# Kernel tuning notes

Hardware: AMD Instinct MI355X
Metric: run time of the kernel (lower is better)

The kernel has to match this reference:

```python
import jax, jax.numpy as jnp
import numpy as np

N_NODES = 50000
N_EDGES = 600000
IN_DIM = 128
HID = 128
OUT_DIM = 40
NUM_REL = 3
LN_EPS = 1e-5


def layer_norm(x, g, b):
    mu = jnp.mean(x, axis=-1, keepdims=True)
    var = jnp.var(x, axis=-1, keepdims=True)
    return (x - mu) * jax.lax.rsqrt(var + LN_EPS) * g + b


def rgcn_conv(x, edge_index, edge_type, w_rel, w_root, bias, aggr):
    """PyG-style RGCNConv: out = x @ W_root + bias + sum_r aggr_r(x_src @ W_r)."""
    src, dst = edge_index[0], edge_index[1]
    out = x @ w_root + bias                      # [N, F_out]
    for r in range(NUM_REL):                     # small fixed relation loop
        h = x @ w_rel[r]                         # transform-then-gather: [N, F_out]
        msg = h[src]                             # [E, F_out]
        mask = (edge_type == r)[:, None]
        if aggr == 'add':
            msg = jnp.where(mask, msg, 0.0)
            agg = jax.ops.segment_sum(msg, dst, num_segments=N_NODES)
        else:  # 'max'; empty segments -> 0 (matches PyG scatter_reduce include_self=False over zeros)
            msg = jnp.where(mask, msg, -jnp.inf)
            agg = jax.ops.segment_max(msg, dst, num_segments=N_NODES)
            agg = jnp.where(jnp.isfinite(agg), agg, 0.0)
        out = out + agg
    return out


def setup_inputs() -> dict:
    key = jax.random.key(0)
    ks = jax.random.split(key, 16)
    f32 = jnp.float32
    def lin(k, fan_in, shape):
        return jax.random.normal(k, shape, dtype=f32) / np.sqrt(fan_in)
    inp = {
        'x': jax.random.normal(ks[0], (N_NODES, IN_DIM), dtype=f32),
        'edge_index': jax.random.randint(ks[1], (2, N_EDGES), 0, N_NODES),
        'edge_type': jax.random.randint(ks[2], (N_EDGES,), 0, NUM_REL),
        # conv1
        'w1_rel': lin(ks[3], IN_DIM, (NUM_REL, IN_DIM, HID)),
        'w1_root': lin(ks[4], IN_DIM, (IN_DIM, HID)),
        'b1': jnp.zeros((HID,), f32),
        'ln1_g': jnp.ones((HID,), f32), 'ln1_b': jnp.zeros((HID,), f32),
        # conv2
        'w2_rel': lin(ks[5], HID, (NUM_REL, HID, HID)),
        'w2_root': lin(ks[6], HID, (HID, HID)),
        'b2': jnp.zeros((HID,), f32),
        'ln2_g': jnp.ones((HID,), f32), 'ln2_b': jnp.zeros((HID,), f32),
        # classifier
        'cw1': lin(ks[7], HID, (HID, HID)), 'cb1': jnp.zeros((HID,), f32),
        'cln1_g': jnp.ones((HID,), f32), 'cln1_b': jnp.zeros((HID,), f32),
        'cw2': lin(ks[8], HID, (HID, HID // 2)), 'cb2': jnp.zeros((HID // 2,), f32),
        'cln2_g': jnp.ones((HID // 2,), f32), 'cln2_b': jnp.zeros((HID // 2,), f32),
        'cw3': lin(ks[9], HID // 2, (HID // 2, OUT_DIM)), 'cb3': jnp.zeros((OUT_DIM,), f32),
    }
    return inp


def reference(x, edge_index, edge_type,
              w1_rel, w1_root, b1, ln1_g, ln1_b,
              w2_rel, w2_root, b2, ln2_g, ln2_b,
              cw1, cb1, cln1_g, cln1_b,
              cw2, cb2, cln2_g, cln2_b,
              cw3, cb3):
    # eval mode: edge dropout and feature dropout are identity
    h = rgcn_conv(x, edge_index, edge_type, w1_rel, w1_root, b1, 'add')
    h = jax.nn.relu(layer_norm(h, ln1_g, ln1_b))
    x1 = h
    h = rgcn_conv(x1, edge_index, edge_type, w2_rel, w2_root, b2, 'max')
    h = jax.nn.relu(layer_norm(h, ln2_g, ln2_b))
    h = h + x1 * 0.2
    # classifier MLP
    h = jax.nn.gelu(layer_norm(h @ cw1 + cb1, cln1_g, cln1_b), approximate=False)
    h = jax.nn.gelu(layer_norm(h @ cw2 + cb2, cln2_g, cln2_b), approximate=False)
    h = h @ cw3 + cb3
    return jax.nn.log_softmax(h, axis=1)
```

## Files before the change

kernel.cpp:

```cpp
#include <hip/hip_runtime.h>
#include <hip/hip_bf16.h>
#include <math.h>


typedef __attribute__((ext_vector_type(8))) short bf16x8;
typedef __attribute__((ext_vector_type(4))) float f32x4;
typedef unsigned short ushort_t;

__device__ __forceinline__ ushort_t bf16rne(float v) {
    unsigned u = __float_as_uint(v);
    return (ushort_t)((u + 0x7FFFu + ((u >> 16) & 1u)) >> 16);
}

__device__ __forceinline__ void split_bf16(float v, ushort_t& h, ushort_t& l) {
    ushort_t hu = bf16rne(v);
    float hf = __uint_as_float((unsigned)hu << 16);
    h = hu;
    l = bf16rne(v - hf);
}

__device__ __forceinline__ float bf2f(unsigned u16) {
    return __uint_as_float(u16 << 16);
}

__device__ __forceinline__ float4 unpack_bf4(uint2 u) {
    return make_float4(bf2f(u.x & 0xFFFFu), bf2f(u.x >> 16),
                       bf2f(u.y & 0xFFFFu), bf2f(u.y >> 16));
}

__device__ __forceinline__ uint2 pack_bf4(float4 v) {
    uint2 o;
    o.x = (unsigned)bf16rne(v.x) | ((unsigned)bf16rne(v.y) << 16);
    o.y = (unsigned)bf16rne(v.z) | ((unsigned)bf16rne(v.w) << 16);
    return o;
}

__device__ __forceinline__ void conv_body128(const float* __restrict__ W,
                                             ushort_t* __restrict__ out,
                                             int idx) {
    constexpr int NCF = 8;
    constexpr size_t PST = (size_t)4 * NCF * 512;
    int l = idx & 63;
    int cf = (idx >> 6) & 7;
    int ks = idx >> 9;
    int col = cf * 16 + (l & 15);
    int k0 = ks * 32 + (l >> 4) * 8;
    size_t base = (((size_t)ks * NCF + cf) * 64 + l) * 8;
#pragma unroll
    for (int j = 0; j < 8; ++j) {
        ushort_t h, lo_;
        split_bf16(W[(size_t)(k0 + j) * 128 + col], h, lo_);
        out[base + j] = h;
        out[PST + base + j] = lo_;
    }
}

__global__ __launch_bounds__(256) void convert_all(
    const float* __restrict__ w1_root, const float* __restrict__ w1_rel,
    const float* __restrict__ w2_root, const float* __restrict__ w2_rel,
    const float* __restrict__ cw1, const float* __restrict__ cw2,
    ushort_t* __restrict__ wfb) {
    int b = blockIdx.x;
    if (b < 72) {
        const float* src;
        int slot;
        if (b < 8)       { slot = 0;              src = w1_root; }
        else if (b < 32) { int r = (b - 8) >> 3;  slot = 1 + r; src = w1_rel + (size_t)r * 16384; }
        else if (b < 40) { slot = 4;              src = w2_root; }
        else if (b < 64) { int r = (b - 40) >> 3; slot = 5 + r; src = w2_rel + (size_t)r * 16384; }
        else             { slot = 8;              src = cw1; }
        int lb = (b < 8) ? b : (b < 32) ? ((b - 8) & 7) : (b < 40) ? (b - 32)
               : (b < 64) ? ((b - 40) & 7) : (b - 64);
        conv_body128(src, wfb + (size_t)slot * 32768, lb * 256 + threadIdx.x);
    } else {
        constexpr int NCF = 4;
        constexpr size_t PST = (size_t)4 * NCF * 512;
        int idx = (b - 72) * 256 + threadIdx.x;
        ushort_t* out = wfb + (size_t)9 * 32768;
        int l = idx & 63;
        int cf = (idx >> 6) & 3;
        int ks = idx >> 8;
        int col = cf * 16 + (l & 15);
        int k0 = ks * 32 + (l >> 4) * 8;
        size_t base = (((size_t)ks * NCF + cf) * 64 + l) * 8;
#pragma unroll
        for (int j = 0; j < 8; ++j) {
            ushort_t h, lo_;
            split_bf16(cw2[(size_t)(k0 + j) * 64 + col], h, lo_);
            out[base + j] = h;
            out[PST + base + j] = lo_;
        }
    }
}

__global__ __launch_bounds__(256) void x2bf(const float* __restrict__ x,
                                            ushort_t* __restrict__ xh, int n4) {
    int g = blockIdx.x * 256 + threadIdx.x;
    if (g >= n4) return;
    float4 v = ((const float4*)x)[g];
    ((uint2*)xh)[g] = pack_bf4(v);
}

template <int NCOL, int NSEG, int FUSE>
__global__ __launch_bounds__(256, 3) void gemm_bf(
    const ushort_t* __restrict__ A0, const ushort_t* __restrict__ A1,
    const ushort_t* __restrict__ A2, const ushort_t* __restrict__ A3,
    const ushort_t* __restrict__ wfrag, const float* __restrict__ bias,
    const float* __restrict__ lng, const float* __restrict__ lnb,
    void* __restrict__ Yv, int M) {
    constexpr int NCF = NCOL / 16;
    constexpr int WF = NCOL / 32;
    constexpr int PST = 4 * NCF * 512;
    constexpr int WSEG = 2 * PST;
    constexpr int RS = NCOL * 4 + 16;
    constexpr int EPB = 64 * RS;
    constexpr int SMEM_BYTES = (EPB > 16384) ? EPB : 16384;
    __shared__ __align__(16) char smem[SMEM_BYTES];
    char (*lds)[8192] = (char(*)[8192])smem;

    const int tid = threadIdx.x;
    const int wv = tid >> 6, lane = tid & 63, l15 = lane & 15, lg = lane >> 4;
    const int rowgrp = wv >> 1, colgrp = wv & 1;
    const int row0 = blockIdx.x * 64;
    const ushort_t* As[4] = {A0, A1, A2, A3};

    f32x4 acc[2][WF];
#pragma unroll
    for (int xf = 0; xf < 2; ++xf)
#pragma unroll
        for (int wf = 0; wf < WF; ++wf) acc[xf][wf] = (f32x4){0.f, 0.f, 0.f, 0.f};

    uint4 regs[2];

    auto LOADSTAGE = [&](int ch) {
        const ushort_t* __restrict__ A = As[ch >> 1];
        int kcb = (ch & 1) * 128;
#pragma unroll
        for (int i = 0; i < 2; ++i) {
            int s = tid + i * 256;
            int r = s >> 3, c16 = s & 7;
            int gr = row0 + r;
            uint4 v = make_uint4(0u, 0u, 0u, 0u);
            if (gr < M)
                v = *(const uint4*)((const char*)A + (size_t)gr * 256 + kcb + c16 * 16);
            regs[i] = v;
        }
    };

    auto WRITESTAGE = [&](int buf) {
        char* L = lds[buf];
#pragma unroll
        for (int i = 0; i < 2; ++i) {
            int s = tid + i * 256;
            int r = s >> 3, c16 = s & 7;
            int byte = (r * 128 + c16 * 16) ^ ((r & 7) << 4);
            *(uint4*)(L + byte) = regs[i];
        }
    };

    auto COMPUTE = [&](int ch, int buf) {
        int seg = ch >> 1, half = ch & 1;
        const ushort_t* __restrict__ ws = wfrag + (size_t)seg * WSEG;
        const char* L = lds[buf];
#pragma unroll
        for (int kk = 0; kk < 2; ++kk) {
            int ks = half * 2 + kk;
            bf16x8 xh[2];
#pragma unroll
            for (int xf = 0; xf < 2; ++xf) {
                int r = rowgrp * 32 + xf * 16 + l15;
                int byte = (r * 128 + kk * 64 + lg * 16) ^ ((r & 7) << 4);
                xh[xf] = *(const bf16x8*)(L + byte);
            }
            bf16x8 wh[WF], wl[WF];
#pragma unroll
            for (int wf = 0; wf < WF; ++wf) {
                size_t off = (((size_t)ks * NCF + colgrp * WF + wf) * 64 + lane) * 8;
                wh[wf] = *(const bf16x8*)(ws + off);
                wl[wf] = *(const bf16x8*)(ws + PST + off);
            }
#pragma unroll
            for (int xf = 0; xf < 2; ++xf)
#pragma unroll
                for (int wf = 0; wf < WF; ++wf) {
                    acc[xf][wf] = __builtin_amdgcn_mfma_f32_16x16x32_bf16(
                        wh[wf], xh[xf], acc[xf][wf], 0, 0, 0);
                    acc[xf][wf] = __builtin_amdgcn_mfma_f32_16x16x32_bf16(
                        wl[wf], xh[xf], acc[xf][wf], 0, 0, 0);
                }
        }
    };

    constexpr int CH = 2 * NSEG;
    LOADSTAGE(0);
    WRITESTAGE(0);
    __syncthreads();
    for (int ch = 0; ch < CH; ++ch) {
        if (ch + 1 < CH) LOADSTAGE(ch + 1);
        COMPUTE(ch, ch & 1);
        __syncthreads();
        if (ch + 1 < CH) WRITESTAGE((ch + 1) & 1);
        __syncthreads();
    }

    {
        float4 bv[WF];
#pragma unroll
        for (int wf = 0; wf < WF; ++wf) {
            int col = colgrp * (NCOL / 2) + wf * 16 + lg * 4;
            bv[wf] = bias ? *(const float4*)(bias + col)
                          : make_float4(0.f, 0.f, 0.f, 0.f);
        }
#pragma unroll
        for (int xf = 0; xf < 2; ++xf) {
            int r = rowgrp * 32 + xf * 16 + l15;
#pragma unroll
            for (int wf = 0; wf < WF; ++wf) {
                int col = colgrp * (NCOL / 2) + wf * 16 + lg * 4;
                float4 o;
                o.x = acc[xf][wf][0] + bv[wf].x;
                o.y = acc[xf][wf][1] + bv[wf].y;
                o.z = acc[xf][wf][2] + bv[wf].z;
                o.w = acc[xf][wf][3] + bv[wf].w;
                *(float4*)(smem + r * RS + col * 4) = o;
            }
        }
    }
    __syncthreads();

    if (FUSE >= 1 && FUSE <= 3) {
        constexpr int CPT = NCOL / 4;
        int r = tid >> 2, seg = tid & 3;
        char* rp = smem + r * RS + seg * CPT * 4;
        float s = 0.f, sq = 0.f;
        float4 vv[CPT / 4];
#pragma unroll
        for (int j = 0; j < CPT / 4; ++j) {
            float4 v = *(const float4*)(rp + j * 16);
            vv[j] = v;
            s += (v.x + v.y) + (v.z + v.w);
            sq += (v.x * v.x + v.y * v.y) + (v.z * v.z + v.w * v.w);
        }
        s += __shfl_xor(s, 1, 64); sq += __shfl_xor(sq, 1, 64);
        s += __shfl_xor(s, 2, 64); sq += __shfl_xor(sq, 2, 64);
        float mu = s * (1.f / NCOL);
        float var = sq * (1.f / NCOL) - mu * mu;
        float rstd = rsqrtf(var + 1e-5f);
#pragma unroll
        for (int j = 0; j < CPT / 4; ++j) {
            int c0 = seg * CPT + j * 4;
            float4 v = vv[j];
            float4 gg = *(const float4*)(lng + c0);
            float4 bb = *(const float4*)(lnb + c0);
            float y0 = (v.x - mu) * rstd * gg.x + bb.x;
            float y1 = (v.y - mu) * rstd * gg.y + bb.y;
            float y2 = (v.z - mu) * rstd * gg.z + bb.z;
            float y3 = (v.w - mu) * rstd * gg.w + bb.w;
            if (FUSE == 1) {
                y0 = fmaxf(y0, 0.f); y1 = fmaxf(y1, 0.f);
                y2 = fmaxf(y2, 0.f); y3 = fmaxf(y3, 0.f);
            } else {
                y0 = 0.5f * y0 * (1.f + erff(y0 * 0.70710678118654752f));
                y1 = 0.5f * y1 * (1.f + erff(y1 * 0.70710678118654752f));
                y2 = 0.5f * y2 * (1.f + erff(y2 * 0.70710678118654752f));
                y3 = 0.5f * y3 * (1.f + erff(y3 * 0.70710678118654752f));
            }
            vv[j] = make_float4(y0, y1, y2, y3);
        }
        __syncthreads();
        if (FUSE == 3) {
#pragma unroll
            for (int j = 0; j < CPT / 4; ++j) *(float4*)(rp + j * 16) = vv[j];
        } else {
#pragma unroll
            for (int j = 0; j < CPT / 4; ++j) {
                int c0 = seg * CPT + j * 4;
                *(uint2*)(smem + r * RS + 2 * c0) = pack_bf4(vv[j]);
            }
        }
        __syncthreads();
    }

    if (FUSE == 4) {
        constexpr int SL = 64 * (NCOL / 8);
#pragma unroll
        for (int i = 0; i < SL / 256; ++i) {
            int slot = tid + i * 256;
            int rr = slot / (NCOL / 8), c16 = slot % (NCOL / 8);
            int gr = row0 + rr;
            if (gr < M) {
                float4 a = *(const float4*)(smem + rr * RS + c16 * 32);
                float4 b = *(const float4*)(smem + rr * RS + c16 * 32 + 16);
                uint4 o;
                uint2 pa = pack_bf4(a), pb = pack_bf4(b);
                o.x = pa.x; o.y = pa.y; o.z = pb.x; o.w = pb.y;
                *(uint4*)((char*)Yv + (size_t)gr * (NCOL * 2) + c16 * 16) = o;
            }
        }
    } else {
        constexpr int OUTB = (FUSE == 0 || FUSE == 3) ? NCOL * 4 : NCOL * 2;
        constexpr int RP = OUTB / 16;
        constexpr int SL = 64 * RP;
#pragma unroll
        for (int i = 0; i < SL / 256; ++i) {
            int slot = tid + i * 256;
            int rr = slot / RP, c16 = slot % RP;
            int gr = row0 + rr;
            if (gr < M)
                *(uint4*)((char*)Yv + (size_t)gr * OUTB + c16 * 16) =
                    *(const uint4*)(smem + rr * RS + c16 * 16);
        }
    }
}

__global__ __launch_bounds__(256, 3) void gemm_conv2(
    const ushort_t* __restrict__ X, const ushort_t* __restrict__ wfb,
    const float* __restrict__ b2, ushort_t* __restrict__ ACbf,
    ushort_t* __restrict__ H0, ushort_t* __restrict__ H1,
    ushort_t* __restrict__ H2, int M) {
    constexpr int NCF = 8, WF = 4;
    constexpr int PST = 4 * NCF * 512;
    constexpr int RS2 = 256 + 16;
    __shared__ __align__(16) char smem[16384 + 64 * RS2];
    char* Xs = smem;
    char* ep = smem + 16384;

    const int tid = threadIdx.x;
    const int wv = tid >> 6, lane = tid & 63, l15 = lane & 15, lg = lane >> 4;
    const int rowgrp = wv >> 1, colgrp = wv & 1;
    const int row0 = blockIdx.x * 64;

#pragma unroll
    for (int i = 0; i < 4; ++i) {
        int s = tid + i * 256;
        int r = s >> 4, c16 = s & 15;
        int gr = row0 + r;
        uint4 v = make_uint4(0u, 0u, 0u, 0u);
        if (gr < M) v = *(const uint4*)((const char*)X + (size_t)gr * 256 + c16 * 16);
        int byte = (r * 256 + c16 * 16) ^ ((r & 7) << 4);
        *(uint4*)(Xs + byte) = v;
    }
    __syncthreads();

    ushort_t* outs[4] = {ACbf, H0, H1, H2};
    for (int set = 0; set < 4; ++set) {
        const ushort_t* __restrict__ ws = wfb + (size_t)(4 + set) * 32768;
        f32x4 acc[2][WF];
#pragma unroll
        for (int xf = 0; xf < 2; ++xf)
#pragma unroll
            for (int wf = 0; wf < WF; ++wf) acc[xf][wf] = (f32x4){0.f, 0.f, 0.f, 0.f};
#pragma unroll
        for (int ks = 0; ks < 4; ++ks) {
            bf16x8 xh[2];
#pragma unroll
            for (int xf = 0; xf < 2; ++xf) {
                int r = rowgrp * 32 + xf * 16 + l15;
                int byte = (r * 256 + ks * 64 + lg * 16) ^ ((r & 7) << 4);
                xh[xf] = *(const bf16x8*)(Xs + byte);
            }
            bf16x8 wh[WF], wl[WF];
#pragma unroll
            for (int wf = 0; wf < WF; ++wf) {
                size_t off = (((size_t)ks * NCF + colgrp * WF + wf) * 64 + lane) * 8;
                wh[wf] = *(const bf16x8*)(ws + off);
                wl[wf] = *(const bf16x8*)(ws + PST + off);
            }
#pragma unroll
            for (int xf = 0; xf < 2; ++xf)
#pragma unroll
                for (int wf = 0; wf < WF; ++wf) {
                    acc[xf][wf] = __builtin_amdgcn_mfma_f32_16x16x32_bf16(
                        wh[wf], xh[xf], acc[xf][wf], 0, 0, 0);
                    acc[xf][wf] = __builtin_amdgcn_mfma_f32_16x16x32_bf16(
                        wl[wf], xh[xf], acc[xf][wf], 0, 0, 0);
                }
        }
        __syncthreads();
#pragma unroll
        for (int xf = 0; xf < 2; ++xf) {
            int r = rowgrp * 32 + xf * 16 + l15;
#pragma unroll
            for (int wf = 0; wf < WF; ++wf) {
                int col = colgrp * 64 + wf * 16 + lg * 4;
                float4 o;
                o.x = acc[xf][wf][0];
                o.y = acc[xf][wf][1];
                o.z = acc[xf][wf][2];
                o.w = acc[xf][wf][3];
                if (set == 0) {
                    float4 bv = *(const float4*)(b2 + col);
                    o.x += bv.x; o.y += bv.y; o.z += bv.z; o.w += bv.w;
                }
                *(uint2*)(ep + r * RS2 + col * 2) = pack_bf4(o);
            }
        }
        __syncthreads();
        ushort_t* O = outs[set];
#pragma unroll
        for (int i = 0; i < 4; ++i) {
            int slot = tid + i * 256;
            int rr = slot >> 4, c16 = slot & 15;
            int gr = row0 + rr;
            if (gr < M)
                *(uint4*)((char*)O + (size_t)gr * 256 + c16 * 16) =
                    *(const uint4*)(ep + rr * RS2 + c16 * 16);
        }
    }
}

__global__ __launch_bounds__(256) void hist3_kernel(const int* __restrict__ edst,
                                                    const int* __restrict__ etype,
                                                    int* __restrict__ deg3, int E) {
    int e = blockIdx.x * 256 + threadIdx.x;
    if (e < E) atomicAdd(&deg3[edst[e] * 3 + etype[e]], 1);
}

__global__ __launch_bounds__(256) void degtot_kernel(const int* __restrict__ deg3,
                                                     int* __restrict__ degtot, int N) {
    int n = blockIdx.x * 256 + threadIdx.x;
    if (n < N) degtot[n] = deg3[n * 3] + deg3[n * 3 + 1] + deg3[n * 3 + 2];
}

__global__ __launch_bounds__(256) void scan_block(const int* __restrict__ in,
                                                  int* __restrict__ out,
                                                  int* __restrict__ sums, int n) {
    __shared__ int s[256];
    int g = blockIdx.x * 256 + threadIdx.x;
    int v = (g < n) ? in[g] : 0;
    s[threadIdx.x] = v;
    __syncthreads();
    int acc = v;
    for (int off = 1; off < 256; off <<= 1) {
        int t = (threadIdx.x >= off) ? s[threadIdx.x - off] : 0;
        __syncthreads();
        acc += t;
        s[threadIdx.x] = acc;
        __syncthreads();
    }
    if (g < n) out[g] = acc - v;
    if (threadIdx.x == 255 && sums) sums[blockIdx.x] = acc;
}

__global__ __launch_bounds__(256) void scan_add(int* __restrict__ out,
                                                const int* __restrict__ topex,
                                                int n, int total) {
    int g = blockIdx.x * 256 + threadIdx.x;
    if (g < n) out[g] += topex[blockIdx.x];
    if (g == 0) out[n] = total;
}

__global__ __launch_bounds__(256) void ranges_kernel(
    const int* __restrict__ rowptr, const int* __restrict__ deg3,
    int4* __restrict__ ranges, int* __restrict__ cursor3, int N) {
    int n = blockIdx.x * 256 + threadIdx.x;
    if (n >= N) return;
    int b = rowptr[n];
    int d0 = deg3[n * 3], d1 = deg3[n * 3 + 1];
    int4 r;
    r.x = b; r.y = b + d0; r.z = b + d0 + d1; r.w = rowptr[n + 1];
    ranges[n] = r;
    cursor3[n * 3] = r.x; cursor3[n * 3 + 1] = r.y; cursor3[n * 3 + 2] = r.z;
}

__global__ __launch_bounds__(256) void fill3_kernel(
    const int* __restrict__ esrc, const int* __restrict__ edst,
    const int* __restrict__ etype, int* __restrict__ cursor3,
    int* __restrict__ colidx, int E) {
    int e = blockIdx.x * 256 + threadIdx.x;
    if (e >= E) return;
    int pos = atomicAdd(&cursor3[edst[e] * 3 + etype[e]], 1);
    colidx[pos] = esrc[e];
}

__device__ __forceinline__ float4 gather_sum_bf(const ushort_t* __restrict__ XH,
                                                const int* __restrict__ colidx,
                                                int beg, int end, int l) {
    float4 a = make_float4(0.f, 0.f, 0.f, 0.f);
    int e = beg;
    for (; e + 4 <= end; e += 4) {
        int s0 = colidx[e], s1 = colidx[e + 1];
        int s2 = colidx[e + 2], s3 = colidx[e + 3];
        float4 v0 = unpack_bf4(*(const uint2*)(XH + (size_t)s0 * 128 + l * 4));
        float4 v1 = unpack_bf4(*(const uint2*)(XH + (size_t)s1 * 128 + l * 4));
        float4 v2 = unpack_bf4(*(const uint2*)(XH + (size_t)s2 * 128 + l * 4));
        float4 v3 = unpack_bf4(*(const uint2*)(XH + (size_t)s3 * 128 + l * 4));
        a.x += (v0.x + v1.x) + (v2.x + v3.x);
        a.y += (v0.y + v1.y) + (v2.y + v3.y);
        a.z += (v0.z + v1.z) + (v2.z + v3.z);
        a.w += (v0.w + v1.w) + (v2.w + v3.w);
    }
    for (; e < end; ++e) {
        float4 v = unpack_bf4(*(const uint2*)(XH + (size_t)colidx[e] * 128 + l * 4));
        a.x += v.x; a.y += v.y; a.z += v.z; a.w += v.w;
    }
    return a;
}

__global__ __launch_bounds__(256) void agg3_add(
    const ushort_t* __restrict__ xh, const int4* __restrict__ ranges,
    const int* __restrict__ colidx, ushort_t* __restrict__ S0,
    ushort_t* __restrict__ S1, ushort_t* __restrict__ S2, int N) {
    int node = blockIdx.x * 8 + (threadIdx.x >> 5);
    int l = threadIdx.x & 31;
    if (node >= N) return;
    int4 rg = ranges[node];
    float4 a0 = gather_sum_bf(xh, colidx, rg.x, rg.y, l);
    float4 a1 = gather_sum_bf(xh, colidx, rg.y, rg.z, l);
    float4 a2 = gather_sum_bf(xh, colidx, rg.z, rg.w, l);
    *(uint2*)(S0 + (size_t)node * 128 + l * 4) = pack_bf4(a0);
    *(uint2*)(S1 + (size_t)node * 128 + l * 4) = pack_bf4(a1);
    *(uint2*)(S2 + (size_t)node * 128 + l * 4) = pack_bf4(a2);
}

__device__ __forceinline__ float4 gather_max_bf(const ushort_t* __restrict__ H,
                                                const int* __restrict__ colidx,
                                                int beg, int end, int l) {
    float4 m = make_float4(-INFINITY, -INFINITY, -INFINITY, -INFINITY);
    int e = beg;
    for (; e + 4 <= end; e += 4) {
        int s0 = colidx[e], s1 = colidx[e + 1];
        int s2 = colidx[e + 2], s3 = colidx[e + 3];
        float4 v0 = unpack_bf4(*(const uint2*)(H + (size_t)s0 * 128 + l * 4));
        float4 v1 = unpack_bf4(*(const uint2*)(H + (size_t)s1 * 128 + l * 4));
        float4 v2 = unpack_bf4(*(const uint2*)(H + (size_t)s2 * 128 + l * 4));
        float4 v3 = unpack_bf4(*(const uint2*)(H + (size_t)s3 * 128 + l * 4));
        m.x = fmaxf(m.x, fmaxf(fmaxf(v0.x, v1.x), fmaxf(v2.x, v3.x)));
        m.y = fmaxf(m.y, fmaxf(fmaxf(v0.y, v1.y), fmaxf(v2.y, v3.y)));
        m.z = fmaxf(m.z, fmaxf(fmaxf(v0.z, v1.z), fmaxf(v2.z, v3.z)));
        m.w = fmaxf(m.w, fmaxf(fmaxf(v0.w, v1.w), fmaxf(v2.w, v3.w)));
    }
    for (; e < end; ++e) {
        float4 v = unpack_bf4(*(const uint2*)(H + (size_t)colidx[e] * 128 + l * 4));
        m.x = fmaxf(m.x, v.x); m.y = fmaxf(m.y, v.y);
        m.z = fmaxf(m.z, v.z); m.w = fmaxf(m.w, v.w);
    }
    m.x = (m.x > -3e38f) ? m.x : 0.f;
    m.y = (m.y > -3e38f) ? m.y : 0.f;
    m.z = (m.z > -3e38f) ? m.z : 0.f;
    m.w = (m.w > -3e38f) ? m.w : 0.f;
    return m;
}

__global__ __launch_bounds__(256) void maxagg_ln(
    const ushort_t* __restrict__ H0, const ushort_t* __restrict__ H1,
    const ushort_t* __restrict__ H2, const int4* __restrict__ ranges,
    const int* __restrict__ colidx, const ushort_t* __restrict__ accbf,
    const ushort_t* __restrict__ resid, const float* __restrict__ g,
    const float* __restrict__ b, ushort_t* __restrict__ outH, int N) {
    int node = blockIdx.x * 8 + (threadIdx.x >> 5);
    int l = threadIdx.x & 31;
    if (node >= N) return;
    int4 rg = ranges[node];
    float4 m0 = gather_max_bf(H0, colidx, rg.x, rg.y, l);
    float4 m1 = gather_max_bf(H1, colidx, rg.y, rg.z, l);
    float4 m2 = gather_max_bf(H2, colidx, rg.z, rg.w, l);
    float4 a = unpack_bf4(*(const uint2*)(accbf + (size_t)node * 128 + l * 4));
    a.x += m0.x + m1.x + m2.x;
    a.y += m0.y + m1.y + m2.y;
    a.z += m0.z + m1.z + m2.z;
    a.w += m0.w + m1.w + m2.w;
    float s = (a.x + a.y) + (a.z + a.w);
    float sq = (a.x * a.x + a.y * a.y) + (a.z * a.z + a.w * a.w);
#pragma unroll
    for (int off = 16; off; off >>= 1) {
        s += __shfl_xor(s, off, 64);
        sq += __shfl_xor(sq, off, 64);
    }
    float mu = s * (1.f / 128.f);
    float var = sq * (1.f / 128.f) - mu * mu;
    float rstd = rsqrtf(var + 1e-5f);
    float4 gg = *(const float4*)(g + l * 4);
    float4 bb = *(const float4*)(b + l * 4);
    float4 rv = unpack_bf4(*(const uint2*)(resid + (size_t)node * 128 + l * 4));
    float4 y;
    y.x = fmaxf((a.x - mu) * rstd * gg.x + bb.x, 0.f) + 0.2f * rv.x;
    y.y = fmaxf((a.y - mu) * rstd * gg.y + bb.y, 0.f) + 0.2f * rv.y;
    y.z = fmaxf((a.z - mu) * rstd * gg.z + bb.z, 0.f) + 0.2f * rv.z;
    y.w = fmaxf((a.w - mu) * rstd * gg.w + bb.w, 0.f) + 0.2f * rv.w;
    *(uint2*)(outH + (size_t)node * 128 + l * 4) = pack_bf4(y);
}

__global__ __launch_bounds__(256) void gemm40_lsm(const float* __restrict__ X,
                                                  const float* __restrict__ W,
                                                  const float* __restrict__ bias,
                                                  float* __restrict__ Y, int M) {
    __shared__ float Xs[64][65];
    __shared__ float Ws[64 * 40];
    __shared__ float Ys[64][41];
    __shared__ float mx_[64], ls_[64];
    const int tid = threadIdx.x;
    const int row0 = blockIdx.x * 64;
    for (int i = tid; i < 64 * 40; i += 256) Ws[i] = W[i];
#pragma unroll
    for (int i = 0; i < 4; ++i) {
        int slot = tid + i * 256;
        int r = slot >> 4, c4 = slot & 15;
        float4 v = make_float4(0.f, 0.f, 0.f, 0.f);
        if (row0 + r < M) v = *(const float4*)(X + (size_t)(row0 + r) * 64 + c4 * 4);
        Xs[r][c4 * 4 + 0] = v.x; Xs[r][c4 * 4 + 1] = v.y;
        Xs[r][c4 * 4 + 2] = v.z; Xs[r][c4 * 4 + 3] = v.w;
    }
    __syncthreads();
    const int row = tid >> 2, cg = (tid & 3) * 10;
    float acc[10];
#pragma unroll
    for (int j = 0; j < 10; ++j) acc[j] = 0.f;
#pragma unroll 8
    for (int k = 0; k < 64; ++k) {
        float xv = Xs[row][k];
#pragma unroll
        for (int j = 0; j < 10; ++j) acc[j] = fmaf(xv, Ws[k * 40 + cg + j], acc[j]);
    }
#pragma unroll
    for (int j = 0; j < 10; ++j) Ys[row][cg + j] = acc[j] + bias[cg + j];
    __syncthreads();
    if (tid < 64) {
        float mx = -INFINITY;
#pragma unroll 8
        for (int c = 0; c < 40; ++c) mx = fmaxf(mx, Ys[tid][c]);
        float sum = 0.f;
#pragma unroll 8
        for (int c = 0; c < 40; ++c) sum += __expf(Ys[tid][c] - mx);
        mx_[tid] = mx;
        ls_[tid] = logf(sum);
    }
    __syncthreads();
#pragma unroll
    for (int i = 0; i < 10; ++i) {
        int slot = tid + i * 256;
        int r = slot / 40, c = slot % 40;
        int gr = row0 + r;
        if (gr < M) Y[(size_t)gr * 40 + c] = Ys[r][c] - mx_[r] - ls_[r];
    }
}

extern "C" void kernel_launch(void* const* d_in, const int* in_sizes, int n_in,
                              void* d_out, int out_size, void* d_ws, size_t ws_size,
                              hipStream_t stream) {
    const float* x       = (const float*)d_in[0];
    const int*   eidx    = (const int*)d_in[1];
    const int*   etype   = (const int*)d_in[2];
    const float* w1_rel  = (const float*)d_in[3];
    const float* w1_root = (const float*)d_in[4];
    const float* b1      = (const float*)d_in[5];
    const float* ln1_g   = (const float*)d_in[6];
    const float* ln1_b   = (const float*)d_in[7];
    const float* w2_rel  = (const float*)d_in[8];
    const float* w2_root = (const float*)d_in[9];
    const float* b2      = (const float*)d_in[10];
    const float* ln2_g   = (const float*)d_in[11];
    const float* ln2_b   = (const float*)d_in[12];
    const float* cw1     = (const float*)d_in[13];
    const float* cb1     = (const float*)d_in[14];
    const float* cln1_g  = (const float*)d_in[15];
    const float* cln1_b  = (const float*)d_in[16];
    const float* cw2     = (const float*)d_in[17];
    const float* cb2     = (const float*)d_in[18];
    const float* cln2_g  = (const float*)d_in[19];
    const float* cln2_b  = (const float*)d_in[20];
    const float* cw3     = (const float*)d_in[21];
    const float* cb3     = (const float*)d_in[22];

    const int N = in_sizes[0] / 128;
    const int E = in_sizes[1] / 2;
    const int* esrc = eidx;
    const int* edst = eidx + E;

    const size_t HB = (size_t)N * 256;
    char* base = (char*)d_ws;
    ushort_t* S0 = (ushort_t*)(base + 0 * HB);
    ushort_t* S1 = (ushort_t*)(base + 1 * HB);
    ushort_t* S2 = (ushort_t*)(base + 2 * HB);
    ushort_t* X1 = (ushort_t*)(base + 3 * HB);
    ushort_t* AC = (ushort_t*)(base + 4 * HB);
    char*     B3 = base + 5 * HB;

    int* rowptr  = (int*)B3;
    int* degtot  = rowptr + (N + 1);
    int* deg3    = degtot + N;
    int* cursor3 = deg3 + 3 * N;
    int* bsums   = cursor3 + 3 * N;
    int* btop    = bsums + 256;
    int4* ranges = (int4*)(((uintptr_t)(btop + 256) + 15) & ~(uintptr_t)15);
    int* colidx  = (int*)(ranges + N);
    ushort_t* wfb = (ushort_t*)(((uintptr_t)(colidx + E) + 255) & ~(uintptr_t)255);
    auto WSLOT = [&](int i) { return wfb + (size_t)i * 32768; };
    ushort_t* xh = (ushort_t*)(((uintptr_t)(wfb + 10 * 32768) + 255) & ~(uintptr_t)255);
    ushort_t* h2 = xh;
    ushort_t* C1 = S0;
    float*    C2 = (float*)S1;

    const dim3 blk(256);
    const int gGemm = (N + 63) / 64;
    const int gAgg  = (N + 7) / 8;
    const int gEdge = (E + 255) / 256;
    const int gNode = (N + 255) / 256;
    const int nScanB = (N + 255) / 256;
    const int gX2  = (N * 32 + 255) / 256;

    hipMemsetAsync(deg3, 0, (size_t)3 * N * sizeof(int), stream);
    hist3_kernel<<<gEdge, blk, 0, stream>>>(edst, etype, deg3, E);
    degtot_kernel<<<gNode, blk, 0, stream>>>(deg3, degtot, N);
    scan_block<<<nScanB, blk, 0, stream>>>(degtot, rowptr, bsums, N);
    scan_block<<<1, blk, 0, stream>>>(bsums, btop, nullptr, nScanB);
    scan_add<<<nScanB, blk, 0, stream>>>(rowptr, btop, N, E);
    ranges_kernel<<<gNode, blk, 0, stream>>>(rowptr, deg3, ranges, cursor3, N);
    fill3_kernel<<<gEdge, blk, 0, stream>>>(esrc, edst, etype, cursor3, colidx, E);

    convert_all<<<76, blk, 0, stream>>>(w1_root, w1_rel, w2_root, w2_rel,
                                        cw1, cw2, wfb);
    x2bf<<<gX2, blk, 0, stream>>>(x, xh, N * 32);

    agg3_add<<<gAgg, blk, 0, stream>>>(xh, ranges, colidx, S0, S1, S2, N);
    gemm_bf<128, 4, 1><<<gGemm, blk, 0, stream>>>(
        xh, S0, S1, S2, WSLOT(0), b1, ln1_g, ln1_b, X1, N);

    gemm_conv2<<<gGemm, blk, 0, stream>>>(X1, wfb, b2, AC, S0, S1, S2, N);
    maxagg_ln<<<gAgg, blk, 0, stream>>>(S0, S1, S2, ranges, colidx, AC,
                                        X1, ln2_g, ln2_b, h2, N);

    gemm_bf<128, 1, 2><<<gGemm, blk, 0, stream>>>(
        h2, h2, h2, h2, WSLOT(8), cb1, cln1_g, cln1_b, C1, N);
    gemm_bf<64, 1, 3><<<gGemm, blk, 0, stream>>>(
        C1, C1, C1, C1, WSLOT(9), cb2, cln2_g, cln2_b, C2, N);
    gemm40_lsm<<<gGemm, blk, 0, stream>>>(C2, cw3, cb3, (float*)d_out, N);
}
```

Measured before the change: 266.9 us.

## Fuse CSR-build and conversion kernels; merge per-relation gathers into one 8-wide loop

Folds the degree sum into the block scan, merges scan_add with the ranges kernel, and merges weight conversion with the x-to-bf16 cast, which removes several small launches. The add and max aggregation kernels now walk a node's whole edge range in a single loop with 8 loads in flight, using predicates to route each edge to its relation's accumulator. The aim is more memory-level parallelism and fewer short loops per node. Max aggregation assumes S0, S1 and S2 are contiguous with stride N*128, and the predicated accumulation costs extra ALU work per edge.

```diff
diff --git a/kernel.cpp b/kernel.cpp
--- a/kernel.cpp
+++ b/kernel.cpp
@@ -55,12 +55,21 @@
     }
 }
 
-__global__ __launch_bounds__(256) void convert_all(
+__global__ __launch_bounds__(256) void convert_all_x2bf(
     const float* __restrict__ w1_root, const float* __restrict__ w1_rel,
     const float* __restrict__ w2_root, const float* __restrict__ w2_rel,
     const float* __restrict__ cw1, const float* __restrict__ cw2,
-    ushort_t* __restrict__ wfb) {
+    ushort_t* __restrict__ wfb,
+    const float* __restrict__ x, ushort_t* __restrict__ xh, int n4) {
     int b = blockIdx.x;
+    if (b >= 76) {
+        int g = (b - 76) * 256 + threadIdx.x;
+        if (g < n4) {
+            float4 v = ((const float4*)x)[g];
+            ((uint2*)xh)[g] = pack_bf4(v);
+        }
+        return;
+    }
     if (b < 72) {
         const float* src;
         int slot;
@@ -93,14 +102,6 @@
     }
 }
 
-__global__ __launch_bounds__(256) void x2bf(const float* __restrict__ x,
-                                            ushort_t* __restrict__ xh, int n4) {
-    int g = blockIdx.x * 256 + threadIdx.x;
-    if (g >= n4) return;
-    float4 v = ((const float4*)x)[g];
-    ((uint2*)xh)[g] = pack_bf4(v);
-}
-
 template <int NCOL, int NSEG, int FUSE>
 __global__ __launch_bounds__(256, 3) void gemm_bf(
     const ushort_t* __restrict__ A0, const ushort_t* __restrict__ A1,
@@ -416,10 +417,25 @@
     if (e < E) atomicAdd(&deg3[edst[e] * 3 + etype[e]], 1);
 }
 
-__global__ __launch_bounds__(256) void degtot_kernel(const int* __restrict__ deg3,
-                                                     int* __restrict__ degtot, int N) {
-    int n = blockIdx.x * 256 + threadIdx.x;
-    if (n < N) degtot[n] = deg3[n * 3] + deg3[n * 3 + 1] + deg3[n * 3 + 2];
+__global__ __launch_bounds__(256) void scan_deg3(const int* __restrict__ deg3,
+                                                 int* __restrict__ out,
+                                                 int* __restrict__ sums, int n) {
+    __shared__ int s[256];
+    int g = blockIdx.x * 256 + threadIdx.x;
+    int v = 0;
+    if (g < n) v = deg3[g * 3] + deg3[g * 3 + 1] + deg3[g * 3 + 2];
+    s[threadIdx.x] = v;
+    __syncthreads();
+    int acc = v;
+    for (int off = 1; off < 256; off <<= 1) {
+        int t = (threadIdx.x >= off) ? s[threadIdx.x - off] : 0;
+        __syncthreads();
+        acc += t;
+        s[threadIdx.x] = acc;
+        __syncthreads();
+    }
+    if (g < n) out[g] = acc - v;
+    if (threadIdx.x == 255 && sums) sums[blockIdx.x] = acc;
 }
 
 __global__ __launch_bounds__(256) void scan_block(const int* __restrict__ in,
@@ -442,25 +458,18 @@
     if (threadIdx.x == 255 && sums) sums[blockIdx.x] = acc;
 }
 
-__global__ __launch_bounds__(256) void scan_add(int* __restrict__ out,
-                                                const int* __restrict__ topex,
-                                                int n, int total) {
+__global__ __launch_bounds__(256) void scan_add_ranges(
+    const int* __restrict__ scanned, const int* __restrict__ topex,
+    const int* __restrict__ deg3, int4* __restrict__ ranges,
+    int* __restrict__ cursor3, int n) {
     int g = blockIdx.x * 256 + threadIdx.x;
-    if (g < n) out[g] += topex[blockIdx.x];
-    if (g == 0) out[n] = total;
-}
-
-__global__ __launch_bounds__(256) void ranges_kernel(
-    const int* __restrict__ rowptr, const int* __restrict__ deg3,
-    int4* __restrict__ ranges, int* __restrict__ cursor3, int N) {
-    int n = blockIdx.x * 256 + threadIdx.x;
-    if (n >= N) return;
-    int b = rowptr[n];
-    int d0 = deg3[n * 3], d1 = deg3[n * 3 + 1];
+    if (g >= n) return;
+    int b = scanned[g] + topex[blockIdx.x];
+    int d0 = deg3[g * 3], d1 = deg3[g * 3 + 1], d2 = deg3[g * 3 + 2];
     int4 r;
-    r.x = b; r.y = b + d0; r.z = b + d0 + d1; r.w = rowptr[n + 1];
-    ranges[n] = r;
-    cursor3[n * 3] = r.x; cursor3[n * 3 + 1] = r.y; cursor3[n * 3 + 2] = r.z;
+    r.x = b; r.y = b + d0; r.z = b + d0 + d1; r.w = b + d0 + d1 + d2;
+    ranges[g] = r;
+    cursor3[g * 3] = r.x; cursor3[g * 3 + 1] = r.y; cursor3[g * 3 + 2] = r.z;
 }
 
 __global__ __launch_bounds__(256) void fill3_kernel(
@@ -473,30 +482,6 @@
     colidx[pos] = esrc[e];
 }
 
-__device__ __forceinline__ float4 gather_sum_bf(const ushort_t* __restrict__ XH,
-                                                const int* __restrict__ colidx,
-                                                int beg, int end, int l) {
-    float4 a = make_float4(0.f, 0.f, 0.f, 0.f);
-    int e = beg;
-    for (; e + 4 <= end; e += 4) {
-        int s0 = colidx[e], s1 = colidx[e + 1];
-        int s2 = colidx[e + 2], s3 = colidx[e + 3];
-        float4 v0 = unpack_bf4(*(const uint2*)(XH + (size_t)s0 * 128 + l * 4));
-        float4 v1 = unpack_bf4(*(const uint2*)(XH + (size_t)s1 * 128 + l * 4));
-        float4 v2 = unpack_bf4(*(const uint2*)(XH + (size_t)s2 * 128 + l * 4));
-        float4 v3 = unpack_bf4(*(const uint2*)(XH + (size_t)s3 * 128 + l * 4));
-        a.x += (v0.x + v1.x) + (v2.x + v3.x);
-        a.y += (v0.y + v1.y) + (v2.y + v3.y);
-        a.z += (v0.z + v1.z) + (v2.z + v3.z);
-        a.w += (v0.w + v1.w) + (v2.w + v3.w);
-    }
-    for (; e < end; ++e) {
-        float4 v = unpack_bf4(*(const uint2*)(XH + (size_t)colidx[e] * 128 + l * 4));
-        a.x += v.x; a.y += v.y; a.z += v.z; a.w += v.w;
-    }
-    return a;
-}
-
 __global__ __launch_bounds__(256) void agg3_add(
     const ushort_t* __restrict__ xh, const int4* __restrict__ ranges,
     const int* __restrict__ colidx, ushort_t* __restrict__ S0,
@@ -505,46 +490,56 @@
     int l = threadIdx.x & 31;
     if (node >= N) return;
     int4 rg = ranges[node];
-    float4 a0 = gather_sum_bf(xh, colidx, rg.x, rg.y, l);
-    float4 a1 = gather_sum_bf(xh, colidx, rg.y, rg.z, l);
-    float4 a2 = gather_sum_bf(xh, colidx, rg.z, rg.w, l);
+    float4 a0 = make_float4(0.f, 0.f, 0.f, 0.f);
+    float4 a1 = a0, a2 = a0;
+    int e = rg.x, end = rg.w;
+
+    auto acc1 = [&](int ee, uint2 u) {
+        float4 v = unpack_bf4(u);
+        bool i0 = ee < rg.y;
+        bool i2 = ee >= rg.z;
+        bool i1 = !i0 && !i2;
+        a0.x += i0 ? v.x : 0.f; a0.y += i0 ? v.y : 0.f;
+        a0.z += i0 ? v.z : 0.f; a0.w += i0 ? v.w : 0.f;
+        a1.x += i1 ? v.x : 0.f; a1.y += i1 ? v.y : 0.f;
+        a1.z += i1 ? v.z : 0.f; a1.w += i1 ? v.w : 0.f;
+        a2.x += i2 ? v.x : 0.f; a2.y += i2 ? v.y : 0.f;
+        a2.z += i2 ? v.z : 0.f; a2.w += i2 ? v.w : 0.f;
+    };
+
+    for (; e + 8 <= end; e += 8) {
+        int s[8];
+#pragma unroll
+        for (int k = 0; k < 8; ++k) s[k] = colidx[e + k];
+        uint2 u[8];
+#pragma unroll
+        for (int k = 0; k < 8; ++k)
+            u[k] = *(const uint2*)(xh + (size_t)s[k] * 128 + l * 4);
+#pragma unroll
+        for (int k = 0; k < 8; ++k) acc1(e + k, u[k]);
+    }
+    if (e + 4 <= end) {
+        int s[4];
+#pragma unroll
+        for (int k = 0; k < 4; ++k) s[k] = colidx[e + k];
+        uint2 u[4];
+#pragma unroll
+        for (int k = 0; k < 4; ++k)
+            u[k] = *(const uint2*)(xh + (size_t)s[k] * 128 + l * 4);
+#pragma unroll
+        for (int k = 0; k < 4; ++k) acc1(e + k, u[k]);
+        e += 4;
+    }
+    for (; e < end; ++e)
+        acc1(e, *(const uint2*)(xh + (size_t)colidx[e] * 128 + l * 4));
+
     *(uint2*)(S0 + (size_t)node * 128 + l * 4) = pack_bf4(a0);
     *(uint2*)(S1 + (size_t)node * 128 + l * 4) = pack_bf4(a1);
     *(uint2*)(S2 + (size_t)node * 128 + l * 4) = pack_bf4(a2);
 }
 
-__device__ __forceinline__ float4 gather_max_bf(const ushort_t* __restrict__ H,
-                                                const int* __restrict__ colidx,
-                                                int beg, int end, int l) {
-    float4 m = make_float4(-INFINITY, -INFINITY, -INFINITY, -INFINITY);
-    int e = beg;
-    for (; e + 4 <= end; e += 4) {
-        int s0 = colidx[e], s1 = colidx[e + 1];
-        int s2 = colidx[e + 2], s3 = colidx[e + 3];
-        float4 v0 = unpack_bf4(*(const uint2*)(H + (size_t)s0 * 128 + l * 4));
-        float4 v1 = unpack_bf4(*(const uint2*)(H + (size_t)s1 * 128 + l * 4));
-        float4 v2 = unpack_bf4(*(const uint2*)(H + (size_t)s2 * 128 + l * 4));
-        float4 v3 = unpack_bf4(*(const uint2*)(H + (size_t)s3 * 128 + l * 4));
-        m.x = fmaxf(m.x, fmaxf(fmaxf(v0.x, v1.x), fmaxf(v2.x, v3.x)));
-        m.y = fmaxf(m.y, fmaxf(fmaxf(v0.y, v1.y), fmaxf(v2.y, v3.y)));
-        m.z = fmaxf(m.z, fmaxf(fmaxf(v0.z, v1.z), fmaxf(v2.z, v3.z)));
-        m.w = fmaxf(m.w, fmaxf(fmaxf(v0.w, v1.w), fmaxf(v2.w, v3.w)));
-    }
-    for (; e < end; ++e) {
-        float4 v = unpack_bf4(*(const uint2*)(H + (size_t)colidx[e] * 128 + l * 4));
-        m.x = fmaxf(m.x, v.x); m.y = fmaxf(m.y, v.y);
-        m.z = fmaxf(m.z, v.z); m.w = fmaxf(m.w, v.w);
-    }
-    m.x = (m.x > -3e38f) ? m.x : 0.f;
-    m.y = (m.y > -3e38f) ? m.y : 0.f;
-    m.z = (m.z > -3e38f) ? m.z : 0.f;
-    m.w = (m.w > -3e38f) ? m.w : 0.f;
-    return m;
-}
-
 __global__ __launch_bounds__(256) void maxagg_ln(
-    const ushort_t* __restrict__ H0, const ushort_t* __restrict__ H1,
-    const ushort_t* __restrict__ H2, const int4* __restrict__ ranges,
+    const ushort_t* __restrict__ Hbase, const int4* __restrict__ ranges,
     const int* __restrict__ colidx, const ushort_t* __restrict__ accbf,
     const ushort_t* __restrict__ resid, const float* __restrict__ g,
     const float* __restrict__ b, ushort_t* __restrict__ outH, int N) {
@@ -552,9 +547,59 @@
     int l = threadIdx.x & 31;
     if (node >= N) return;
     int4 rg = ranges[node];
-    float4 m0 = gather_max_bf(H0, colidx, rg.x, rg.y, l);
-    float4 m1 = gather_max_bf(H1, colidx, rg.y, rg.z, l);
-    float4 m2 = gather_max_bf(H2, colidx, rg.z, rg.w, l);
+    const float NI = -INFINITY;
+    float4 m0 = make_float4(NI, NI, NI, NI);
+    float4 m1 = m0, m2 = m0;
+    int e = rg.x, end = rg.w;
+
+    auto acc1 = [&](int ee, uint2 u) {
+        float4 v = unpack_bf4(u);
+        bool i0 = ee < rg.y;
+        bool i2 = ee >= rg.z;
+        bool i1 = !i0 && !i2;
+        m0.x = fmaxf(m0.x, i0 ? v.x : NI); m0.y = fmaxf(m0.y, i0 ? v.y : NI);
+        m0.z = fmaxf(m0.z, i0 ? v.z : NI); m0.w = fmaxf(m0.w, i0 ? v.w : NI);
+        m1.x = fmaxf(m1.x, i1 ? v.x : NI); m1.y = fmaxf(m1.y, i1 ? v.y : NI);
+        m1.z = fmaxf(m1.z, i1 ? v.z : NI); m1.w = fmaxf(m1.w, i1 ? v.w : NI);
+        m2.x = fmaxf(m2.x, i2 ? v.x : NI); m2.y = fmaxf(m2.y, i2 ? v.y : NI);
+        m2.z = fmaxf(m2.z, i2 ? v.z : NI); m2.w = fmaxf(m2.w, i2 ? v.w : NI);
+    };
+    auto addr = [&](int ee, int src) {
+        int rel = (ee >= rg.y) + (ee >= rg.z);
+        return Hbase + ((size_t)rel * N + src) * 128 + l * 4;
+    };
+
+    for (; e + 8 <= end; e += 8) {
+        int s[8];
+#pragma unroll
+        for (int k = 0; k < 8; ++k) s[k] = colidx[e + k];
+        uint2 u[8];
+#pragma unroll
+        for (int k = 0; k < 8; ++k) u[k] = *(const uint2*)addr(e + k, s[k]);
+#pragma unroll
+        for (int k = 0; k < 8; ++k) acc1(e + k, u[k]);
+    }
+    if (e + 4 <= end) {
+        int s[4];
+#pragma unroll
+        for (int k = 0; k < 4; ++k) s[k] = colidx[e + k];
+        uint2 u[4];
+#pragma unroll
+        for (int k = 0; k < 4; ++k) u[k] = *(const uint2*)(addr(e + k, s[k]));
+#pragma unroll
+        for (int k = 0; k < 4; ++k) acc1(e + k, u[k]);
+        e += 4;
+    }
+    for (; e < end; ++e) acc1(e, *(const uint2*)addr(e, colidx[e]));
+
+    auto fix = [](float4& m) {
+        m.x = (m.x > -3e38f) ? m.x : 0.f;
+        m.y = (m.y > -3e38f) ? m.y : 0.f;
+        m.z = (m.z > -3e38f) ? m.z : 0.f;
+        m.w = (m.w > -3e38f) ? m.w : 0.f;
+    };
+    fix(m0); fix(m1); fix(m2);
+
     float4 a = unpack_bf4(*(const uint2*)(accbf + (size_t)node * 128 + l * 4));
     a.x += m0.x + m1.x + m2.x;
     a.y += m0.y + m1.y + m2.y;
@@ -677,8 +722,7 @@
     char*     B3 = base + 5 * HB;
 
     int* rowptr  = (int*)B3;
-    int* degtot  = rowptr + (N + 1);
-    int* deg3    = degtot + N;
+    int* deg3    = rowptr + (N + 1);
     int* cursor3 = deg3 + 3 * N;
     int* bsums   = cursor3 + 3 * N;
     int* btop    = bsums + 256;
@@ -695,29 +739,26 @@
     const int gGemm = (N + 63) / 64;
     const int gAgg  = (N + 7) / 8;
     const int gEdge = (E + 255) / 256;
-    const int gNode = (N + 255) / 256;
     const int nScanB = (N + 255) / 256;
     const int gX2  = (N * 32 + 255) / 256;
 
     hipMemsetAsync(deg3, 0, (size_t)3 * N * sizeof(int), stream);
     hist3_kernel<<<gEdge, blk, 0, stream>>>(edst, etype, deg3, E);
-    degtot_kernel<<<gNode, blk, 0, stream>>>(deg3, degtot, N);
-    scan_block<<<nScanB, blk, 0, stream>>>(degtot, rowptr, bsums, N);
+    scan_deg3<<<nScanB, blk, 0, stream>>>(deg3, rowptr, bsums, N);
     scan_block<<<1, blk, 0, stream>>>(bsums, btop, nullptr, nScanB);
-    scan_add<<<nScanB, blk, 0, stream>>>(rowptr, btop, N, E);
-    ranges_kernel<<<gNode, blk, 0, stream>>>(rowptr, deg3, ranges, cursor3, N);
+    scan_add_ranges<<<nScanB, blk, 0, stream>>>(rowptr, btop, deg3, ranges,
+                                                cursor3, N);
     fill3_kernel<<<gEdge, blk, 0, stream>>>(esrc, edst, etype, cursor3, colidx, E);
 
-    convert_all<<<76, blk, 0, stream>>>(w1_root, w1_rel, w2_root, w2_rel,
-                                        cw1, cw2, wfb);
-    x2bf<<<gX2, blk, 0, stream>>>(x, xh, N * 32);
+    convert_all_x2bf<<<76 + gX2, blk, 0, stream>>>(
+        w1_root, w1_rel, w2_root, w2_rel, cw1, cw2, wfb, x, xh, N * 32);
 
     agg3_add<<<gAgg, blk, 0, stream>>>(xh, ranges, colidx, S0, S1, S2, N);
     gemm_bf<128, 4, 1><<<gGemm, blk, 0, stream>>>(
         xh, S0, S1, S2, WSLOT(0), b1, ln1_g, ln1_b, X1, N);
 
     gemm_conv2<<<gGemm, blk, 0, stream>>>(X1, wfb, b2, AC, S0, S1, S2, N);
-    maxagg_ln<<<gAgg, blk, 0, stream>>>(S0, S1, S2, ranges, colidx, AC,
+    maxagg_ln<<<gAgg, blk, 0, stream>>>(S0, ranges, colidx, AC,
                                         X1, ln2_g, ln2_b, h2, N);
 
     gemm_bf<128, 1, 2><<<gGemm, blk, 0, stream>>>(
```

Result: faster. 257.7 us, median of 2 (-3.4%).
